# Performance work log

Hardware: AMD Instinct MI355X
Metric: run time of the kernel (lower is better)

Reference implementation:

```python
import jax, jax.numpy as jnp
import numpy as np

B, V, C, G, D, H, W, N = 1, 4, 32, 8, 8, 240, 320, 9
EPS = 1e-5  # BatchNorm3d default eps


def grid_sample(img, grid, align_corners, zeros_pad):
    # img [B,C,Hs,Ws], grid [B,Hg,Wg,2] normalized coords; mirrors torch F.grid_sample bilinear
    Bi, Ci, Hs, Ws = img.shape
    gx, gy = grid[..., 0], grid[..., 1]
    if align_corners:
        ix = (gx + 1.0) * 0.5 * (Ws - 1)
        iy = (gy + 1.0) * 0.5 * (Hs - 1)
    else:
        ix = ((gx + 1.0) * Ws - 1.0) * 0.5
        iy = ((gy + 1.0) * Hs - 1.0) * 0.5
    x0 = jnp.floor(ix)
    y0 = jnp.floor(iy)
    wx1 = ix - x0
    wy1 = iy - y0

    def corner(xi, yi, wgt):
        xc = jnp.clip(xi, 0, Ws - 1).astype(jnp.int32)
        yc = jnp.clip(yi, 0, Hs - 1).astype(jnp.int32)
        v = jax.vmap(lambda im, yy, xx: im[:, yy, xx])(img, yc, xc)  # [B,C,Hg,Wg]
        if zeros_pad:
            valid = ((xi >= 0) & (xi <= Ws - 1) & (yi >= 0) & (yi <= Hs - 1)).astype(img.dtype)
            wgt = wgt * valid
        return v * wgt[:, None]

    return (corner(x0, y0, (1 - wx1) * (1 - wy1)) + corner(x0 + 1, y0, wx1 * (1 - wy1))
            + corner(x0, y0 + 1, (1 - wx1) * wy1) + corner(x0 + 1, y0 + 1, wx1 * wy1))


def differentiable_warping(src_fea, src_proj, ref_proj, depth):
    # src_fea [B,Cf,H,W], projs [B,4,4], depth [B,D,H,W] -> [B,Cf,D,H,W]
    Bi, Cf, Hs, Ws = src_fea.shape
    Dd = depth.shape[1]
    proj = src_proj @ jnp.linalg.inv(ref_proj)
    rot, trans = proj[:, :3, :3], proj[:, :3, 3:4]
    yy, xx = jnp.meshgrid(jnp.arange(Hs, dtype=jnp.float32), jnp.arange(Ws, dtype=jnp.float32), indexing='ij')
    xyz = jnp.stack([xx.ravel(), yy.ravel(), jnp.ones(Hs * Ws, jnp.float32)], axis=0)  # [3,HW]
    rot_xyz = jnp.einsum('bij,jk->bik', rot, xyz)  # [B,3,HW]
    pxyz = rot_xyz[:, :, None, :] * depth.reshape(Bi, 1, Dd, Hs * Ws) + trans[:, :, :, None]  # [B,3,D,HW]
    neg = pxyz[:, 2] <= 1e-3
    px = jnp.where(neg, float(Ws), pxyz[:, 0])
    py = jnp.where(neg, float(Hs), pxyz[:, 1])
    pz = jnp.where(neg, 1.0, pxyz[:, 2])
    gx = (px / pz) / ((Ws - 1) / 2.0) - 1.0
    gy = (py / pz) / ((Hs - 1) / 2.0) - 1.0
    grid = jnp.stack([gx, gy], axis=-1).reshape(Bi, Dd * Hs, Ws, 2)
    grid = jax.lax.stop_gradient(grid)  # torch builds the warp grid under no_grad
    warped = grid_sample(src_fea, grid, align_corners=True, zeros_pad=True)  # [B,Cf,D*H,W]
    return warped.reshape(Bi, Cf, Dd, Hs, Ws)


def conv_bn_relu(x, w, bn):
    # 1x1x1 Conv3d (no bias) + BatchNorm3d (inference) + ReLU; x [B,Ci,D,H,W]
    y = jnp.einsum('oi,bidhw->bodhw', w, x)
    g, b, m, v = bn
    s = g / jnp.sqrt(v + EPS)
    return jax.nn.relu(y * s[:, None, None, None] + (b - m * s)[:, None, None, None])


def conv1(x, w, b):
    return jnp.einsum('oi,bidhw->bodhw', w, x) + b[:, None, None, None]


def pixel_wise_net(sim, w0, bn0, w1, bn1, w2, b2):
    y = conv_bn_relu(sim, w0, bn0)
    y = conv_bn_relu(y, w1, bn1)
    y = jax.nn.sigmoid(conv1(y, w2, b2))[:, 0]  # [B,D,H,W]
    return jnp.max(y, axis=1, keepdims=True)  # [B,1,H,W]


def _forward(ref_feature, src_features, ref_proj, src_projs, depth_sample, grid, weight,
             pw_w0, pw_bn0, pw_w1, pw_bn1, pw_w2, pw_b2,
             sn_w0, sn_bn0, sn_w1, sn_bn1, sn_w2, sn_b2):
    Bi, Cf, Hs, Ws = ref_feature.shape
    Gq = pw_w0.shape[1]
    Dd = depth_sample.shape[1]
    ref_g = ref_feature.reshape(Bi, Gq, Cf // Gq, 1, Hs, Ws)
    sim_sum = jnp.zeros((Bi, Gq, Dd, Hs, Ws), jnp.float32)
    w_sum = jnp.zeros((Bi, 1, 1, Hs, Ws), jnp.float32)
    vws = []
    for v in range(src_features.shape[0]):  # small fixed view count
        warped = differentiable_warping(src_features[v], src_projs[v], ref_proj, depth_sample)
        warped = warped.reshape(Bi, Gq, Cf // Gq, Dd, Hs, Ws)
        sim = jnp.mean(warped * ref_g, axis=2)  # [B,G,D,H,W] group correlation
        vw = pixel_wise_net(sim, pw_w0, pw_bn0, pw_w1, pw_bn1, pw_w2, pw_b2)  # [B,1,H,W]
        vws.append(vw)
        sim_sum = sim_sum + sim * vw[:, :, None]
        w_sum = w_sum + vw[:, :, None]
    x = sim_sum / w_sum
    # SimilarityNet: conv stack -> neighbor grid_sample -> adaptive weighted sum
    y = conv_bn_relu(x, sn_w0, sn_bn0)
    y = conv_bn_relu(y, sn_w1, sn_bn1)
    y = conv1(y, sn_w2, sn_b2)[:, 0]  # [B,D,H,W]
    s = grid_sample(y, grid, align_corners=False, zeros_pad=False)  # border pad, [B,D,N*H,W]
    Nn = grid.shape[1] // Hs
    s = s.reshape(Bi, Dd, Nn, Hs, Ws)
    score_vol = jnp.sum(s * weight, axis=2)  # [B,D,H,W]
    score = jax.nn.softmax(score_vol, axis=1)  # exp(log_softmax) == softmax
    depth = jnp.sum(depth_sample * score, axis=1)  # [B,H,W] (is_inverse=False)
    view_weights = jax.lax.stop_gradient(jnp.concatenate(vws, axis=1))  # [B,V,H,W]
    return depth, score, view_weights


def setup_inputs():
    key = jax.random.key(0)
    ks = jax.random.split(key, 20)
    ref_feature = jax.random.normal(ks[0], (B, C, H, W), jnp.float32)
    src_features = jax.random.normal(ks[1], (V, B, C, H, W), jnp.float32)
    f = 500.0
    K = np.array([[f, 0, W / 2.0, 0], [0, f, H / 2.0, 0], [0, 0, 1, 0], [0, 0, 0, 1]], np.float32)
    ref_proj = jnp.asarray(np.tile(K[None], (B, 1, 1)))
    sp = []
    for tx, ty in [(20.0, 0.0), (-20.0, 0.0), (0.0, 10.0), (0.0, -10.0)]:
        E = np.eye(4, dtype=np.float32)
        E[0, 3], E[1, 3] = tx, ty
        sp.append(np.tile((K @ E)[None], (B, 1, 1)))
    src_projs = jnp.asarray(np.stack(sp))
    depth_sample = jnp.sort(425.0 + 510.0 * jax.random.uniform(ks[2], (B, D, H, W), jnp.float32), axis=1)
    # evaluation neighbor grid: per-pixel +-3px learned-style offsets, align_corners=False normalization
    dx = jax.random.uniform(ks[3], (B, N, H, W), minval=-3.0, maxval=3.0)
    dy = jax.random.uniform(ks[4], (B, N, H, W), minval=-3.0, maxval=3.0)
    xs = jnp.arange(W, dtype=jnp.float32)[None, None, None, :]
    ys = jnp.arange(H, dtype=jnp.float32)[None, None, :, None]
    gx = (2.0 * (xs + dx) + 1.0) / W - 1.0
    gy = (2.0 * (ys + dy) + 1.0) / H - 1.0
    grid = jnp.stack([gx, gy], -1).reshape(B, N * H, W, 2)
    weight = jax.random.uniform(ks[5], (B, D, N, H, W), jnp.float32)  # feature*depth weight in (0,1)

    def bn(k, c):
        k1, k2, k3, k4 = jax.random.split(k, 4)
        return jnp.stack([1.0 + 0.1 * jax.random.normal(k1, (c,)), 0.1 * jax.random.normal(k2, (c,)),
                          0.01 * jax.random.normal(k3, (c,)), 1.0 + 0.1 * jax.random.uniform(k4, (c,))])

    return dict(ref_feature=ref_feature, src_features=src_features, ref_proj=ref_proj,
                src_projs=src_projs, depth_sample=depth_sample, grid=grid, weight=weight,
                pw_w0=0.1 * jax.random.normal(ks[6], (16, G)), pw_bn0=bn(ks[7], 16),
                pw_w1=0.1 * jax.random.normal(ks[8], (8, 16)), pw_bn1=bn(ks[9], 8),
                pw_w2=0.1 * jax.random.normal(ks[10], (1, 8)), pw_b2=jnp.zeros((1,), jnp.float32),
                sn_w0=0.1 * jax.random.normal(ks[11], (16, G)), sn_bn0=bn(ks[12], 16),
                sn_w1=0.1 * jax.random.normal(ks[13], (8, 16)), sn_bn1=bn(ks[14], 8),
                sn_w2=0.1 * jax.random.normal(ks[15], (1, 8)), sn_b2=jnp.zeros((1,), jnp.float32))


def reference(ref_feature, src_features, ref_proj, src_projs, depth_sample, grid, weight,
              pw_w0, pw_bn0, pw_w1, pw_bn1, pw_w2, pw_b2,
              sn_w0, sn_bn0, sn_w1, sn_bn1, sn_w2, sn_b2):
    return _forward(ref_feature, src_features, ref_proj, src_projs, depth_sample, grid, weight,
                    pw_w0, pw_bn0, pw_w1, pw_bn1, pw_w2, pw_b2,
                    sn_w0, sn_bn0, sn_w1, sn_bn1, sn_w2, sn_b2)
```

## Files before the change

kernel.cpp:

```cpp
#include <hip/hip_runtime.h>
#include <hip/hip_fp16.h>
#include <cstdint>
#include <cstddef>

#define HH 240
#define WW 320
#define HWPIX 76800
#define NVIEW 4
#define NCH 32
#define NGRP 8
#define NDEP 8
#define NNEI 9
#define SPLANE (HWPIX * NCH)

#define OFF_PROJ 0
#define OFF_PW   48
#define OFF_SN   208
#define OFF_Y    640
#define OFF_SRCT 615040
#define OFF_DEPT (OFF_SRCT + 5 * SPLANE / 2)

typedef _Float16 h2 __attribute__((ext_vector_type(2)));

__device__ __forceinline__ float fdot2_(h2 a, h2 b, float c) {
#if __has_builtin(__builtin_amdgcn_fdot2)
  return __builtin_amdgcn_fdot2(a, b, c, false);
#else
  return c + (float)a.x * (float)b.x + (float)a.y * (float)b.y;
#endif
}
__device__ __forceinline__ h2 pk_(float a, float b) {
#if __has_builtin(__builtin_amdgcn_cvt_pkrtz)
  return __builtin_bit_cast(h2, __builtin_amdgcn_cvt_pkrtz(a, b));
#else
  h2 r; r.x = (_Float16)a; r.y = (_Float16)b; return r;
#endif
}

__device__ __forceinline__ float maxd8(float x) {
  int xi = __builtin_bit_cast(int, x);
  int t = __builtin_amdgcn_mov_dpp(xi, 0xB1, 0xF, 0xF, true);
  x = fmaxf(x, __builtin_bit_cast(float, t));
  xi = __builtin_bit_cast(int, x);
  t = __builtin_amdgcn_mov_dpp(xi, 0x4E, 0xF, 0xF, true);
  x = fmaxf(x, __builtin_bit_cast(float, t));
  xi = __builtin_bit_cast(int, x);
  int a = __builtin_amdgcn_update_dpp(xi, xi, 0x124, 0xF, 0x5, false);
  int b = __builtin_amdgcn_update_dpp(a,  xi, 0x12C, 0xF, 0xA, false);
  x = fmaxf(x, __builtin_bit_cast(float, b));
  return x;
}

__device__ __forceinline__ float mlp_h(const float* __restrict__ p, const h2 x[4]) {
  const h2* w0 = (const h2*)p;
  const h2* w1 = (const h2*)(p + 64);
  const h2* w2 = (const h2*)(p + 128);
  h2 hx[8];
#pragma unroll
  for (int o = 0; o < 8; ++o) {
    float a0 = p[132 + 2 * o], a1 = p[132 + 2 * o + 1];
#pragma unroll
    for (int i = 0; i < 4; ++i) {
      a0 = fdot2_(w0[(2 * o) * 4 + i], x[i], a0);
      a1 = fdot2_(w0[(2 * o + 1) * 4 + i], x[i], a1);
    }
    hx[o] = pk_(fmaxf(a0, 0.0f), fmaxf(a1, 0.0f));
  }
  h2 hy[4];
#pragma unroll
  for (int o = 0; o < 4; ++o) {
    float a0 = p[148 + 2 * o], a1 = p[148 + 2 * o + 1];
#pragma unroll
    for (int i = 0; i < 8; ++i) {
      a0 = fdot2_(w1[(2 * o) * 8 + i], hx[i], a0);
      a1 = fdot2_(w1[(2 * o + 1) * 8 + i], hx[i], a1);
    }
    hy[o] = pk_(fmaxf(a0, 0.0f), fmaxf(a1, 0.0f));
  }
  float acc = p[156];
#pragma unroll
  for (int i = 0; i < 4; ++i) acc = fdot2_(w2[i], hy[i], acc);
  return acc;
}

__global__ void k_setup(const float* __restrict__ refP, const float* __restrict__ srcP,
                        const float* __restrict__ pw0, const float* __restrict__ pbn0,
                        const float* __restrict__ pw1, const float* __restrict__ pbn1,
                        const float* __restrict__ pw2, const float* __restrict__ pb2,
                        const float* __restrict__ sw0, const float* __restrict__ sbn0,
                        const float* __restrict__ sw1, const float* __restrict__ sbn1,
                        const float* __restrict__ sw2, const float* __restrict__ sb2,
                        float* __restrict__ ws) {
  int tid = threadIdx.x;
  if (tid == 578) {
    float a[4][8];
    for (int i = 0; i < 4; ++i)
      for (int j = 0; j < 4; ++j) { a[i][j] = refP[i * 4 + j]; a[i][4 + j] = (i == j) ? 1.0f : 0.0f; }
    for (int c = 0; c < 4; ++c) {
      int piv = c; float best = fabsf(a[c][c]);
      for (int r = c + 1; r < 4; ++r) { float t = fabsf(a[r][c]); if (t > best) { best = t; piv = r; } }
      if (piv != c) for (int j = 0; j < 8; ++j) { float t = a[c][j]; a[c][j] = a[piv][j]; a[piv][j] = t; }
      float inv = 1.0f / a[c][c];
      for (int j = 0; j < 8; ++j) a[c][j] *= inv;
      for (int r = 0; r < 4; ++r) if (r != c) {
        float f = a[r][c];
        for (int j = 0; j < 8; ++j) a[r][j] -= f * a[c][j];
      }
    }
    for (int v = 0; v < NVIEW; ++v) {
      const float* S = srcP + v * 16;
      for (int i = 0; i < 3; ++i)
        for (int j = 0; j < 4; ++j) {
          float p = S[i*4+0]*a[0][4+j] + S[i*4+1]*a[1][4+j] + S[i*4+2]*a[2][4+j] + S[i*4+3]*a[3][4+j];
          if (j < 3) ws[v * 12 + i * 3 + j] = p;
          else       ws[v * 12 + 9 + i] = p;
        }
    }
    return;
  }
  if (tid >= 578) return;
  int k = tid / 289;
  int j = tid - k * 289;
  const float* W0 = k ? sw0 : pw0;  const float* B0 = k ? sbn0 : pbn0;
  const float* W1 = k ? sw1 : pw1;  const float* B1 = k ? sbn1 : pbn1;
  const float* W2 = k ? sw2 : pw2;  const float* B2 = k ? sb2 : pb2;
  float* p = ws + (k ? OFF_SN : OFF_PW);
  __half* w0h = (__half*)p;
  __half* w1h = (__half*)(p + 64);
  __half* w2h = (__half*)(p + 128);
  if (j < 128) {
    int o = j >> 3;
    float s = B0[o] / sqrtf(B0[48 + o] + 1e-5f);
    w0h[j] = __float2half_rn(W0[j] * s * 0.25f);
  } else if (j < 256) {
    int idx = j - 128; int o = idx >> 4;
    float s = B1[o] / sqrtf(B1[24 + o] + 1e-5f);
    w1h[idx] = __float2half_rn(W1[idx] * s);
  } else if (j < 264) {
    w2h[j - 256] = __float2half_rn(W2[j - 256]);
  } else if (j < 280) {
    int o = j - 264;
    float s = B0[o] / sqrtf(B0[48 + o] + 1e-5f);
    p[132 + o] = B0[16 + o] - B0[32 + o] * s;
  } else if (j < 288) {
    int o = j - 280;
    float s = B1[o] / sqrtf(B1[24 + o] + 1e-5f);
    p[148 + o] = B1[8 + o] - B1[16 + o] * s;
  } else {
    p[156] = B2[0];
  }
}

__global__ __launch_bounds__(256) void k_transpose(const float* __restrict__ src,
                                                   const float* __restrict__ ref,
                                                   const float* __restrict__ depthS,
                                                   __half* __restrict__ dst,
                                                   float* __restrict__ dep_t, int total) {
  int t = blockIdx.x * 256 + threadIdx.x;
  if (t >= total) return;
  const int base = 5 * HWPIX * 4;
  if (t >= base) {
    int pix = t - base;
    float4 a, b;
    a.x = depthS[0 * HWPIX + pix]; a.y = depthS[1 * HWPIX + pix];
    a.z = depthS[2 * HWPIX + pix]; a.w = depthS[3 * HWPIX + pix];
    b.x = depthS[4 * HWPIX + pix]; b.y = depthS[5 * HWPIX + pix];
    b.z = depthS[6 * HWPIX + pix]; b.w = depthS[7 * HWPIX + pix];
    float4* o = reinterpret_cast<float4*>(dep_t + (size_t)pix * NDEP);
    o[0] = a; o[1] = b;
    return;
  }
  int c8 = t & 3;
  int vp = t >> 2;
  int v = vp / HWPIX;
  int pix = vp - v * HWPIX;
  const float* s = (v < NVIEW) ? (src + ((size_t)(v * NCH + c8 * 8)) * HWPIX + pix)
                               : (ref + ((size_t)(c8 * 8)) * HWPIX + pix);
  union { h2 h[4]; float4 f; } u;
  u.h[0] = pk_(s[0],         s[HWPIX]);
  u.h[1] = pk_(s[2 * HWPIX], s[3 * HWPIX]);
  u.h[2] = pk_(s[4 * HWPIX], s[5 * HWPIX]);
  u.h[3] = pk_(s[6 * HWPIX], s[7 * HWPIX]);
  reinterpret_cast<float4*>(dst + (size_t)vp * NCH)[c8] = u.f;
}

__device__ __forceinline__ void tap_f16(const __half* __restrict__ p, float wtf,
                                        h2 wp[16], bool first) {
  _Float16 wh = (_Float16)wtf;
  h2 wt2 = h2{wh, wh};
  const float4* q = reinterpret_cast<const float4*>(p);
#pragma unroll
  for (int i = 0; i < 4; ++i) {
    union { float4 f; h2 h[4]; } u; u.f = q[i];
#pragma unroll
    for (int c = 0; c < 4; ++c) {
      if (first) wp[4 * i + c] = u.h[c] * wt2;
      else       wp[4 * i + c] += u.h[c] * wt2;
    }
  }
}

template <int MODE>
__global__ __launch_bounds__(256) void k_main(
    const float* __restrict__ ref, const float* __restrict__ src,
    const __half* __restrict__ srcT,
    const float* __restrict__ depthS, const float* __restrict__ dep_t,
    const float* __restrict__ wsc,
    float* __restrict__ ybuf, float* __restrict__ outVW) {
  int t = blockIdx.x * 256 + threadIdx.x;
  int d = t & 7;
  int pix = t >> 3;
  int h = pix / WW;
  int w = pix - h * WW;
  float fx = (float)w, fy = (float)h;

  h2 rc[16];
  float rcf[(MODE == 0) ? NCH : 1];
  if (MODE == 1) {
    const float4* rp = reinterpret_cast<const float4*>(srcT + (size_t)NVIEW * SPLANE + (size_t)pix * NCH);
#pragma unroll
    for (int i = 0; i < 4; ++i) {
      union { float4 f; h2 h[4]; } u; u.f = rp[i];
      rc[4*i] = u.h[0]; rc[4*i+1] = u.h[1]; rc[4*i+2] = u.h[2]; rc[4*i+3] = u.h[3];
    }
  } else {
#pragma unroll
    for (int c = 0; c < NCH; ++c) rcf[c] = ref[c * HWPIX + pix];
  }
  float dep = (MODE == 1) ? dep_t[(size_t)pix * NDEP + d] : depthS[d * HWPIX + pix];

  float ssum[NGRP];
#pragma unroll
  for (int g = 0; g < NGRP; ++g) ssum[g] = 0.0f;
  float wsum = 0.0f;

#pragma unroll 1
  for (int v = 0; v < NVIEW; ++v) {
    const float* pr = wsc + v * 12;
    float rx = fmaf(pr[0], fx, fmaf(pr[1], fy, pr[2]));
    float ry = fmaf(pr[3], fx, fmaf(pr[4], fy, pr[5]));
    float rz = fmaf(pr[6], fx, fmaf(pr[7], fy, pr[8]));
    float pz_ = fmaf(rz, dep, pr[11]);
    bool neg = (pz_ <= 0.001f);
    float px_ = neg ? (float)WW : fmaf(rx, dep, pr[9]);
    float py_ = neg ? (float)HH : fmaf(ry, dep, pr[10]);
    float rpz = neg ? 1.0f : __fdividef(1.0f, pz_);
    float ix = px_ * rpz;
    float iy = py_ * rpz;
    float x0f = floorf(ix), y0f = floorf(iy);
    float wx1 = ix - x0f, wy1 = iy - y0f;
    float wx0 = 1.0f - wx1, wy0 = 1.0f - wy1;
    float x1f = x0f + 1.0f, y1f = y0f + 1.0f;
    float vx0 = (x0f >= 0.0f && x0f <= (float)(WW - 1)) ? 1.0f : 0.0f;
    float vx1 = (x1f >= 0.0f && x1f <= (float)(WW - 1)) ? 1.0f : 0.0f;
    float vy0 = (y0f >= 0.0f && y0f <= (float)(HH - 1)) ? 1.0f : 0.0f;
    float vy1 = (y1f >= 0.0f && y1f <= (float)(HH - 1)) ? 1.0f : 0.0f;
    int xa = (int)fminf(fmaxf(x0f, 0.0f), (float)(WW - 1));
    int xb = (int)fminf(fmaxf(x1f, 0.0f), (float)(WW - 1));
    int ya = (int)fminf(fmaxf(y0f, 0.0f), (float)(HH - 1));
    int yb = (int)fminf(fmaxf(y1f, 0.0f), (float)(HH - 1));
    float w00 = wx0 * wy0 * vx0 * vy0;
    float w01 = wx1 * wy0 * vx1 * vy0;
    float w10 = wx0 * wy1 * vx0 * vy1;
    float w11 = wx1 * wy1 * vx1 * vy1;

    float simf[NGRP];
    if (MODE == 1) {
      const __half* vbase = srcT + (size_t)v * SPLANE;
      h2 wp[16];
      tap_f16(vbase + (size_t)(ya * WW + xa) * NCH, w00, wp, true);
      tap_f16(vbase + (size_t)(ya * WW + xb) * NCH, w01, wp, false);
      tap_f16(vbase + (size_t)(yb * WW + xa) * NCH, w10, wp, false);
      tap_f16(vbase + (size_t)(yb * WW + xb) * NCH, w11, wp, false);
#pragma unroll
      for (int g = 0; g < NGRP; ++g)
        simf[g] = fdot2_(wp[2*g+1], rc[2*g+1], fdot2_(wp[2*g], rc[2*g], 0.0f));
    } else {
      const float* base = src + (size_t)v * NCH * HWPIX;
      const float* p00 = base + ya * WW + xa;
      const float* p01 = base + ya * WW + xb;
      const float* p10 = base + yb * WW + xa;
      const float* p11 = base + yb * WW + xb;
#pragma unroll
      for (int g = 0; g < NGRP; ++g) {
        float acc = 0.0f;
#pragma unroll
        for (int cc = 0; cc < 4; ++cc) {
          size_t o = (size_t)(g * 4 + cc) * HWPIX;
          float wv = w00 * p00[o] + w01 * p01[o] + w10 * p10[o] + w11 * p11[o];
          acc = fmaf(wv, rcf[g * 4 + cc], acc);
        }
        simf[g] = acc;
      }
    }

    h2 x[4];
#pragma unroll
    for (int i = 0; i < 4; ++i) x[i] = pk_(simf[2*i], simf[2*i+1]);
    float sc = mlp_h(wsc + OFF_PW, x);
    sc = maxd8(sc);
    float vw = __fdividef(1.0f, 1.0f + __expf(-sc));
#pragma unroll
    for (int g = 0; g < NGRP; ++g) ssum[g] = fmaf(simf[g], vw, ssum[g]);
    wsum += vw;
    if (d == 0) outVW[v * HWPIX + pix] = vw;
  }

  float rw = __fdividef(1.0f, wsum);
  h2 xg[4];
#pragma unroll
  for (int i = 0; i < 4; ++i) xg[i] = pk_(ssum[2*i] * rw, ssum[2*i+1] * rw);
  float yv = mlp_h(wsc + OFF_SN, xg);
  ybuf[pix * NDEP + d] = yv;
}

__global__ __launch_bounds__(256) void k_score(
    const float* __restrict__ grid, const float* __restrict__ weight,
    const float* __restrict__ depthS, const float* __restrict__ dep_t,
    const float* __restrict__ ybuf, float* __restrict__ out, int useDT) {
  int pix = blockIdx.x * 256 + threadIdx.x;
  int h = pix / WW;
  int w = pix - h * WW;
  float sv[NDEP];
#pragma unroll
  for (int d = 0; d < NDEP; ++d) sv[d] = 0.0f;

#pragma unroll 1
  for (int n = 0; n < NNEI; ++n) {
    int gi = ((n * HH + h) * WW + w) * 2;
    float gx = grid[gi], gy = grid[gi + 1];
    float ix = ((gx + 1.0f) * (float)WW - 1.0f) * 0.5f;
    float iy = ((gy + 1.0f) * (float)HH - 1.0f) * 0.5f;
    float x0f = floorf(ix), y0f = floorf(iy);
    float wx1 = ix - x0f, wy1 = iy - y0f;
    float wx0 = 1.0f - wx1, wy0 = 1.0f - wy1;
    int xa = (int)fminf(fmaxf(x0f, 0.0f), (float)(WW - 1));
    int xb = (int)fminf(fmaxf(x0f + 1.0f, 0.0f), (float)(WW - 1));
    int ya = (int)fminf(fmaxf(y0f, 0.0f), (float)(HH - 1));
    int yb2 = (int)fminf(fmaxf(y0f + 1.0f, 0.0f), (float)(HH - 1));
    const float4* p00 = reinterpret_cast<const float4*>(ybuf + (size_t)(ya * WW + xa) * NDEP);
    const float4* p01 = reinterpret_cast<const float4*>(ybuf + (size_t)(ya * WW + xb) * NDEP);
    const float4* p10 = reinterpret_cast<const float4*>(ybuf + (size_t)(yb2 * WW + xa) * NDEP);
    const float4* p11 = reinterpret_cast<const float4*>(ybuf + (size_t)(yb2 * WW + xb) * NDEP);
    float4 a00 = p00[0], b00 = p00[1];
    float4 a01 = p01[0], b01 = p01[1];
    float4 a10 = p10[0], b10 = p10[1];
    float4 a11 = p11[0], b11 = p11[1];
    const float* v00 = (const float*)&a00;
    const float* v01 = (const float*)&a01;
    const float* v10 = (const float*)&a10;
    const float* v11 = (const float*)&a11;
    const float* u00 = (const float*)&b00;
    const float* u01 = (const float*)&b01;
    const float* u10 = (const float*)&b10;
    const float* u11 = (const float*)&b11;
#pragma unroll
    for (int d = 0; d < NDEP; ++d) {
      float c00 = (d < 4) ? v00[d] : u00[d - 4];
      float c01 = (d < 4) ? v01[d] : u01[d - 4];
      float c10 = (d < 4) ? v10[d] : u10[d - 4];
      float c11 = (d < 4) ? v11[d] : u11[d - 4];
      float s = wy0 * fmaf(wx0, c00, wx1 * c01) + wy1 * fmaf(wx0, c10, wx1 * c11);
      float wn = weight[((size_t)(d * NNEI + n) * HH + h) * WW + w];
      sv[d] = fmaf(s, wn, sv[d]);
    }
  }
  float m = sv[0];
#pragma unroll
  for (int d = 1; d < NDEP; ++d) m = fmaxf(m, sv[d]);
  float e[NDEP], s8 = 0.0f;
#pragma unroll
  for (int d = 0; d < NDEP; ++d) { e[d] = __expf(sv[d] - m); s8 += e[d]; }
  float r = __fdividef(1.0f, s8);
  float dpv[NDEP];
  if (useDT) {
    const float4* dp4 = reinterpret_cast<const float4*>(dep_t + (size_t)pix * NDEP);
    float4 da = dp4[0], db = dp4[1];
    dpv[0]=da.x; dpv[1]=da.y; dpv[2]=da.z; dpv[3]=da.w;
    dpv[4]=db.x; dpv[5]=db.y; dpv[6]=db.z; dpv[7]=db.w;
  } else {
#pragma unroll
    for (int d = 0; d < NDEP; ++d) dpv[d] = depthS[d * HWPIX + pix];
  }
  float dp = 0.0f;
#pragma unroll
  for (int d = 0; d < NDEP; ++d) {
    float sc = e[d] * r;
    out[HWPIX + d * HWPIX + pix] = sc;
    dp = fmaf(dpv[d], sc, dp);
  }
  out[pix] = dp;
}

extern "C" void kernel_launch(void* const* d_in, const int* in_sizes, int n_in,
                              void* d_out, int out_size, void* d_ws, size_t ws_size,
                              hipStream_t stream) {
  const float* ref    = (const float*)d_in[0];
  const float* src    = (const float*)d_in[1];
  const float* refP   = (const float*)d_in[2];
  const float* srcP   = (const float*)d_in[3];
  const float* depthS = (const float*)d_in[4];
  const float* grid   = (const float*)d_in[5];
  const float* weight = (const float*)d_in[6];
  float* out = (float*)d_out;
  float* ws  = (float*)d_ws;
  __half* srcT = (__half*)(ws + OFF_SRCT);
  float* dep_t = ws + OFF_DEPT;

  size_t need = ((size_t)OFF_DEPT + (size_t)NDEP * HWPIX) * 4;
  int mode = (ws_size >= need) ? 1 : 0;

  k_setup<<<1, 640, 0, stream>>>(refP, srcP,
                                 (const float*)d_in[7], (const float*)d_in[8],
                                 (const float*)d_in[9], (const float*)d_in[10],
                                 (const float*)d_in[11], (const float*)d_in[12],
                                 (const float*)d_in[13], (const float*)d_in[14],
                                 (const float*)d_in[15], (const float*)d_in[16],
                                 (const float*)d_in[17], (const float*)d_in[18], ws);
  if (mode == 1) {
    int total = 5 * HWPIX * 4 + HWPIX;
    k_transpose<<<(total + 255) / 256, 256, 0, stream>>>(src, ref, depthS, srcT, dep_t, total);
    k_main<1><<<(HWPIX * 8) / 256, 256, 0, stream>>>(ref, src, srcT, depthS, dep_t, ws,
                                                     ws + OFF_Y, out + 9 * HWPIX);
  } else {
    k_main<0><<<(HWPIX * 8) / 256, 256, 0, stream>>>(ref, src, srcT, depthS, dep_t, ws,
                                                     ws + OFF_Y, out + 9 * HWPIX);
  }
  k_score<<<HWPIX / 256, 256, 0, stream>>>(grid, weight, depthS, dep_t, ws + OFF_Y, out, mode);
}
```

Before: 93.31 us.

## Run per-pixel MLPs on MFMA and merge setup into transpose kernel

Replaces the scalar fdot2-based three-layer MLPs (pixel-wise view weight net and similarity net) with 32x32x16 f16 MFMA instructions. Weight fragments are pre-laid out in the workspace, and half-wave shuffles exchange activations between lanes. The setup kernel is folded into the transpose kernel as an extra block, which removes one launch. The fallback non-transposed path is dropped, so a large workspace is now assumed. The new layout adds shuffle and select overhead, and the MFMA tiles are mostly padding.

```diff
diff --git a/kernel.cpp b/kernel.cpp
--- a/kernel.cpp
+++ b/kernel.cpp
@@ -13,14 +13,14 @@
 #define NNEI 9
 #define SPLANE (HWPIX * NCH)
 
-#define OFF_PROJ 0
-#define OFF_PW   48
-#define OFF_SN   208
-#define OFF_Y    640
-#define OFF_SRCT 615040
-#define OFF_DEPT (OFF_SRCT + 5 * SPLANE / 2)
+#define OFF_TAB 64
+#define OFF_Y    4096
+#define OFF_SRCT 618496
+#define OFF_DEPT 6762496
 
 typedef _Float16 h2 __attribute__((ext_vector_type(2)));
+typedef __fp16  h8v __attribute__((ext_vector_type(8)));
+typedef float f32x16 __attribute__((ext_vector_type(16)));
 
 __device__ __forceinline__ float fdot2_(h2 a, h2 b, float c) {
 #if __has_builtin(__builtin_amdgcn_fdot2)
@@ -35,6 +35,13 @@
 #else
   h2 r; r.x = (_Float16)a; r.y = (_Float16)b; return r;
 #endif
+}
+__device__ __forceinline__ float pkf_(float a, float b) {
+  return __builtin_bit_cast(float, pk_(a, b));
+}
+
+__device__ __forceinline__ f32x16 mfma_(h8v a, h8v b, f32x16 c) {
+  return __builtin_amdgcn_mfma_f32_32x32x16_f16(a, b, c, 0, 0, 0);
 }
 
 __device__ __forceinline__ float maxd8(float x) {
@@ -51,113 +58,145 @@
   return x;
 }
 
-__device__ __forceinline__ float mlp_h(const float* __restrict__ p, const h2 x[4]) {
-  const h2* w0 = (const h2*)p;
-  const h2* w1 = (const h2*)(p + 64);
-  const h2* w2 = (const h2*)(p + 128);
-  h2 hx[8];
-#pragma unroll
-  for (int o = 0; o < 8; ++o) {
-    float a0 = p[132 + 2 * o], a1 = p[132 + 2 * o + 1];
-#pragma unroll
-    for (int i = 0; i < 4; ++i) {
-      a0 = fdot2_(w0[(2 * o) * 4 + i], x[i], a0);
-      a1 = fdot2_(w0[(2 * o + 1) * 4 + i], x[i], a1);
-    }
-    hx[o] = pk_(fmaxf(a0, 0.0f), fmaxf(a1, 0.0f));
-  }
-  h2 hy[4];
-#pragma unroll
-  for (int o = 0; o < 4; ++o) {
-    float a0 = p[148 + 2 * o], a1 = p[148 + 2 * o + 1];
-#pragma unroll
-    for (int i = 0; i < 8; ++i) {
-      a0 = fdot2_(w1[(2 * o) * 8 + i], hx[i], a0);
-      a1 = fdot2_(w1[(2 * o + 1) * 8 + i], hx[i], a1);
-    }
-    hy[o] = pk_(fmaxf(a0, 0.0f), fmaxf(a1, 0.0f));
-  }
-  float acc = p[156];
-#pragma unroll
-  for (int i = 0; i < 4; ++i) acc = fdot2_(w2[i], hy[i], acc);
-  return acc;
-}
-
-__global__ void k_setup(const float* __restrict__ refP, const float* __restrict__ srcP,
-                        const float* __restrict__ pw0, const float* __restrict__ pbn0,
-                        const float* __restrict__ pw1, const float* __restrict__ pbn1,
-                        const float* __restrict__ pw2, const float* __restrict__ pb2,
-                        const float* __restrict__ sw0, const float* __restrict__ sbn0,
-                        const float* __restrict__ sw1, const float* __restrict__ sbn1,
-                        const float* __restrict__ sw2, const float* __restrict__ sb2,
-                        float* __restrict__ ws) {
-  int tid = threadIdx.x;
-  if (tid == 578) {
-    float a[4][8];
-    for (int i = 0; i < 4; ++i)
-      for (int j = 0; j < 4; ++j) { a[i][j] = refP[i * 4 + j]; a[i][4 + j] = (i == j) ? 1.0f : 0.0f; }
-    for (int c = 0; c < 4; ++c) {
-      int piv = c; float best = fabsf(a[c][c]);
-      for (int r = c + 1; r < 4; ++r) { float t = fabsf(a[r][c]); if (t > best) { best = t; piv = r; } }
-      if (piv != c) for (int j = 0; j < 8; ++j) { float t = a[c][j]; a[c][j] = a[piv][j]; a[piv][j] = t; }
-      float inv = 1.0f / a[c][c];
-      for (int j = 0; j < 8; ++j) a[c][j] *= inv;
-      for (int r = 0; r < 4; ++r) if (r != c) {
-        float f = a[r][c];
-        for (int j = 0; j < 8; ++j) a[r][j] -= f * a[c][j];
+__device__ __forceinline__ float mlp_mfma(float4 x4, h8v w0f, h8v w1f,
+                                          float4 b1s, float4 w2s, float b2v,
+                                          bool lo) {
+  f32x16 Z = {};
+  float4 xsw;
+  xsw.x = __shfl_xor(x4.x, 32, 64);
+  xsw.y = __shfl_xor(x4.y, 32, 64);
+  xsw.z = __shfl_xor(x4.z, 32, 64);
+  xsw.w = __shfl_xor(x4.w, 32, 64);
+  float4 cst;
+  cst.x = __builtin_bit_cast(float, 0x00003C00u);
+  cst.y = 0.0f; cst.z = 0.0f; cst.w = 0.0f;
+  float4 blo, bhi;
+  blo.x = lo ? x4.x : cst.x;  blo.y = lo ? x4.y : cst.y;
+  blo.z = lo ? x4.z : cst.z;  blo.w = lo ? x4.w : cst.w;
+  bhi.x = lo ? xsw.x : cst.x; bhi.y = lo ? xsw.y : cst.y;
+  bhi.z = lo ? xsw.z : cst.z; bhi.w = lo ? xsw.w : cst.w;
+
+  float yv0 = 0.0f, yv1 = 0.0f;
+#pragma unroll
+  for (int bb = 0; bb < 2; ++bb) {
+    float4 bin = bb ? bhi : blo;
+    f32x16 acc = mfma_(w0f, __builtin_bit_cast(h8v, bin), Z);
+    float dw0 = pkf_(fmaxf(acc[0], 0.f), fmaxf(acc[1], 0.f));
+    float dw1 = pkf_(fmaxf(acc[2], 0.f), fmaxf(acc[3], 0.f));
+    float dw2 = pkf_(fmaxf(acc[4], 0.f), fmaxf(acc[5], 0.f));
+    float dw3 = pkf_(fmaxf(acc[6], 0.f), fmaxf(acc[7], 0.f));
+    float s0 = __shfl_xor(dw0, 32, 64);
+    float s1 = __shfl_xor(dw1, 32, 64);
+    float s2 = __shfl_xor(dw2, 32, 64);
+    float s3 = __shfl_xor(dw3, 32, 64);
+    float4 bf;
+    bf.x = lo ? dw0 : s2;
+    bf.y = lo ? dw1 : s3;
+    bf.z = lo ? s0 : dw2;
+    bf.w = lo ? s1 : dw3;
+    f32x16 a2 = mfma_(w1f, __builtin_bit_cast(h8v, bf), Z);
+    float p = fmaxf(a2[0] + b1s.x, 0.f) * w2s.x;
+    p = fmaf(fmaxf(a2[1] + b1s.y, 0.f), w2s.y, p);
+    p = fmaf(fmaxf(a2[2] + b1s.z, 0.f), w2s.z, p);
+    p = fmaf(fmaxf(a2[3] + b1s.w, 0.f), w2s.w, p);
+    p += __shfl_xor(p, 32, 64);
+    if (bb) yv1 = p + b2v; else yv0 = p + b2v;
+  }
+  return lo ? yv0 : yv1;
+}
+
+__global__ __launch_bounds__(256) void k_prep(
+    const float* __restrict__ src, const float* __restrict__ ref,
+    const float* __restrict__ depthS,
+    __half* __restrict__ dst, float* __restrict__ dep_t,
+    const float* __restrict__ refP, const float* __restrict__ srcP,
+    const float* __restrict__ pw0, const float* __restrict__ pbn0,
+    const float* __restrict__ pw1, const float* __restrict__ pbn1,
+    const float* __restrict__ pw2, const float* __restrict__ pb2,
+    const float* __restrict__ sw0, const float* __restrict__ sbn0,
+    const float* __restrict__ sw1, const float* __restrict__ sbn1,
+    const float* __restrict__ sw2, const float* __restrict__ sb2,
+    float* __restrict__ ws, int nTransBlocks) {
+  if ((int)blockIdx.x == nTransBlocks) {
+    int tid = threadIdx.x;
+    if (tid < 128) {
+      int net = tid >> 6;
+      int l = tid & 63;
+      int n = l & 31;
+      int hi = l >> 5;
+      const float* W0 = net ? sw0 : pw0;  const float* B0 = net ? sbn0 : pbn0;
+      const float* W1 = net ? sw1 : pw1;  const float* B1 = net ? sbn1 : pbn1;
+      const float* W2 = net ? sw2 : pw2;
+      float* base = ws + OFF_TAB + net * 1024;
+      float4 r;
+      if (hi == 0 && n < 16) {
+        float s = B0[n] / sqrtf(B0[48 + n] + 1e-5f) * 0.25f;
+        r.x = pkf_(W0[n * 8 + 0] * s, W0[n * 8 + 1] * s);
+        r.y = pkf_(W0[n * 8 + 2] * s, W0[n * 8 + 3] * s);
+        r.z = pkf_(W0[n * 8 + 4] * s, W0[n * 8 + 5] * s);
+        r.w = pkf_(W0[n * 8 + 6] * s, W0[n * 8 + 7] * s);
+      } else if (hi == 1 && n < 16) {
+        float s = B0[n] / sqrtf(B0[48 + n] + 1e-5f);
+        float b0f = B0[16 + n] - B0[32 + n] * s;
+        r.x = pkf_(b0f, 0.f); r.y = 0.f; r.z = 0.f; r.w = 0.f;
+      } else { r.x = r.y = r.z = r.w = 0.f; }
+      ((float4*)(base))[l] = r;
+      float4 q;
+      if (n < 8) {
+        float s = B1[n] / sqrtf(B1[24 + n] + 1e-5f);
+        int o = n * 16 + 8 * hi;
+        q.x = pkf_(W1[o + 0] * s, W1[o + 1] * s);
+        q.y = pkf_(W1[o + 2] * s, W1[o + 3] * s);
+        q.z = pkf_(W1[o + 4] * s, W1[o + 5] * s);
+        q.w = pkf_(W1[o + 6] * s, W1[o + 7] * s);
+      } else { q.x = q.y = q.z = q.w = 0.f; }
+      ((float4*)(base + 256))[l] = q;
+      float4 b;
+      {
+        float bb[4];
+        for (int rr = 0; rr < 4; ++rr) {
+          int o = rr + 4 * hi;
+          float s = B1[o] / sqrtf(B1[24 + o] + 1e-5f);
+          bb[rr] = B1[8 + o] - B1[16 + o] * s;
+        }
+        b.x = bb[0]; b.y = bb[1]; b.z = bb[2]; b.w = bb[3];
+      }
+      ((float4*)(base + 512))[l] = b;
+      float4 w2v;
+      w2v.x = W2[0 + 4 * hi]; w2v.y = W2[1 + 4 * hi];
+      w2v.z = W2[2 + 4 * hi]; w2v.w = W2[3 + 4 * hi];
+      ((float4*)(base + 768))[l] = w2v;
+    } else if (tid == 128) {
+      ws[62] = pb2[0];
+      ws[63] = sb2[0];
+    } else if (tid == 129) {
+      float a[4][8];
+      for (int i = 0; i < 4; ++i)
+        for (int j = 0; j < 4; ++j) { a[i][j] = refP[i * 4 + j]; a[i][4 + j] = (i == j) ? 1.0f : 0.0f; }
+      for (int c = 0; c < 4; ++c) {
+        int piv = c; float best = fabsf(a[c][c]);
+        for (int r2 = c + 1; r2 < 4; ++r2) { float t = fabsf(a[r2][c]); if (t > best) { best = t; piv = r2; } }
+        if (piv != c) for (int j = 0; j < 8; ++j) { float t = a[c][j]; a[c][j] = a[piv][j]; a[piv][j] = t; }
+        float inv = 1.0f / a[c][c];
+        for (int j = 0; j < 8; ++j) a[c][j] *= inv;
+        for (int r2 = 0; r2 < 4; ++r2) if (r2 != c) {
+          float f = a[r2][c];
+          for (int j = 0; j < 8; ++j) a[r2][j] -= f * a[c][j];
+        }
+      }
+      for (int v = 0; v < NVIEW; ++v) {
+        const float* S = srcP + v * 16;
+        for (int i = 0; i < 3; ++i)
+          for (int j = 0; j < 4; ++j) {
+            float p = S[i*4+0]*a[0][4+j] + S[i*4+1]*a[1][4+j] + S[i*4+2]*a[2][4+j] + S[i*4+3]*a[3][4+j];
+            if (j < 3) ws[v * 12 + i * 3 + j] = p;
+            else       ws[v * 12 + 9 + i] = p;
+          }
       }
     }
-    for (int v = 0; v < NVIEW; ++v) {
-      const float* S = srcP + v * 16;
-      for (int i = 0; i < 3; ++i)
-        for (int j = 0; j < 4; ++j) {
-          float p = S[i*4+0]*a[0][4+j] + S[i*4+1]*a[1][4+j] + S[i*4+2]*a[2][4+j] + S[i*4+3]*a[3][4+j];
-          if (j < 3) ws[v * 12 + i * 3 + j] = p;
-          else       ws[v * 12 + 9 + i] = p;
-        }
-    }
     return;
   }
-  if (tid >= 578) return;
-  int k = tid / 289;
-  int j = tid - k * 289;
-  const float* W0 = k ? sw0 : pw0;  const float* B0 = k ? sbn0 : pbn0;
-  const float* W1 = k ? sw1 : pw1;  const float* B1 = k ? sbn1 : pbn1;
-  const float* W2 = k ? sw2 : pw2;  const float* B2 = k ? sb2 : pb2;
-  float* p = ws + (k ? OFF_SN : OFF_PW);
-  __half* w0h = (__half*)p;
-  __half* w1h = (__half*)(p + 64);
-  __half* w2h = (__half*)(p + 128);
-  if (j < 128) {
-    int o = j >> 3;
-    float s = B0[o] / sqrtf(B0[48 + o] + 1e-5f);
-    w0h[j] = __float2half_rn(W0[j] * s * 0.25f);
-  } else if (j < 256) {
-    int idx = j - 128; int o = idx >> 4;
-    float s = B1[o] / sqrtf(B1[24 + o] + 1e-5f);
-    w1h[idx] = __float2half_rn(W1[idx] * s);
-  } else if (j < 264) {
-    w2h[j - 256] = __float2half_rn(W2[j - 256]);
-  } else if (j < 280) {
-    int o = j - 264;
-    float s = B0[o] / sqrtf(B0[48 + o] + 1e-5f);
-    p[132 + o] = B0[16 + o] - B0[32 + o] * s;
-  } else if (j < 288) {
-    int o = j - 280;
-    float s = B1[o] / sqrtf(B1[24 + o] + 1e-5f);
-    p[148 + o] = B1[8 + o] - B1[16 + o] * s;
-  } else {
-    p[156] = B2[0];
-  }
-}
-
-__global__ __launch_bounds__(256) void k_transpose(const float* __restrict__ src,
-                                                   const float* __restrict__ ref,
-                                                   const float* __restrict__ depthS,
-                                                   __half* __restrict__ dst,
-                                                   float* __restrict__ dep_t, int total) {
   int t = blockIdx.x * 256 + threadIdx.x;
-  if (t >= total) return;
   const int base = 5 * HWPIX * 4;
   if (t >= base) {
     int pix = t - base;
@@ -200,34 +239,37 @@
   }
 }
 
-template <int MODE>
 __global__ __launch_bounds__(256) void k_main(
-    const float* __restrict__ ref, const float* __restrict__ src,
-    const __half* __restrict__ srcT,
-    const float* __restrict__ depthS, const float* __restrict__ dep_t,
+    const __half* __restrict__ srcT, const float* __restrict__ dep_t,
     const float* __restrict__ wsc,
     float* __restrict__ ybuf, float* __restrict__ outVW) {
   int t = blockIdx.x * 256 + threadIdx.x;
+  int lane = threadIdx.x & 63;
+  bool lo = lane < 32;
   int d = t & 7;
   int pix = t >> 3;
   int h = pix / WW;
   int w = pix - h * WW;
   float fx = (float)w, fy = (float)h;
 
+  const h8v* Tw0p = (const h8v*)(wsc + OFF_TAB);
+  const h8v* Tw1p = (const h8v*)(wsc + OFF_TAB + 256);
+  h8v w0f_pw = Tw0p[lane];
+  h8v w1f_pw = Tw1p[lane];
+  float4 b1s_pw = ((const float4*)(wsc + OFF_TAB + 512))[lane];
+  float4 w2s_pw = ((const float4*)(wsc + OFF_TAB + 768))[lane];
+  float b2_pw = wsc[62];
+
   h2 rc[16];
-  float rcf[(MODE == 0) ? NCH : 1];
-  if (MODE == 1) {
+  {
     const float4* rp = reinterpret_cast<const float4*>(srcT + (size_t)NVIEW * SPLANE + (size_t)pix * NCH);
 #pragma unroll
     for (int i = 0; i < 4; ++i) {
       union { float4 f; h2 h[4]; } u; u.f = rp[i];
       rc[4*i] = u.h[0]; rc[4*i+1] = u.h[1]; rc[4*i+2] = u.h[2]; rc[4*i+3] = u.h[3];
     }
-  } else {
-#pragma unroll
-    for (int c = 0; c < NCH; ++c) rcf[c] = ref[c * HWPIX + pix];
-  }
-  float dep = (MODE == 1) ? dep_t[(size_t)pix * NDEP + d] : depthS[d * HWPIX + pix];
+  }
+  float dep = dep_t[(size_t)pix * NDEP + d];
 
   float ssum[NGRP];
 #pragma unroll
@@ -265,7 +307,7 @@
     float w11 = wx1 * wy1 * vx1 * vy1;
 
     float simf[NGRP];
-    if (MODE == 1) {
+    {
       const __half* vbase = srcT + (size_t)v * SPLANE;
       h2 wp[16];
       tap_f16(vbase + (size_t)(ya * WW + xa) * NCH, w00, wp, true);
@@ -275,29 +317,14 @@
 #pragma unroll
       for (int g = 0; g < NGRP; ++g)
         simf[g] = fdot2_(wp[2*g+1], rc[2*g+1], fdot2_(wp[2*g], rc[2*g], 0.0f));
-    } else {
-      const float* base = src + (size_t)v * NCH * HWPIX;
-      const float* p00 = base + ya * WW + xa;
-      const float* p01 = base + ya * WW + xb;
-      const float* p10 = base + yb * WW + xa;
-      const float* p11 = base + yb * WW + xb;
-#pragma unroll
-      for (int g = 0; g < NGRP; ++g) {
-        float acc = 0.0f;
-#pragma unroll
-        for (int cc = 0; cc < 4; ++cc) {
-          size_t o = (size_t)(g * 4 + cc) * HWPIX;
-          float wv = w00 * p00[o] + w01 * p01[o] + w10 * p10[o] + w11 * p11[o];
-          acc = fmaf(wv, rcf[g * 4 + cc], acc);
-        }
-        simf[g] = acc;
-      }
     }
 
-    h2 x[4];
-#pragma unroll
-    for (int i = 0; i < 4; ++i) x[i] = pk_(simf[2*i], simf[2*i+1]);
-    float sc = mlp_h(wsc + OFF_PW, x);
+    float4 xp;
+    xp.x = pkf_(simf[0], simf[1]);
+    xp.y = pkf_(simf[2], simf[3]);
+    xp.z = pkf_(simf[4], simf[5]);
+    xp.w = pkf_(simf[6], simf[7]);
+    float sc = mlp_mfma(xp, w0f_pw, w1f_pw, b1s_pw, w2s_pw, b2_pw, lo);
     sc = maxd8(sc);
     float vw = __fdividef(1.0f, 1.0f + __expf(-sc));
 #pragma unroll
@@ -307,17 +334,24 @@
   }
 
   float rw = __fdividef(1.0f, wsum);
-  h2 xg[4];
-#pragma unroll
-  for (int i = 0; i < 4; ++i) xg[i] = pk_(ssum[2*i] * rw, ssum[2*i+1] * rw);
-  float yv = mlp_h(wsc + OFF_SN, xg);
+  float4 xg;
+  xg.x = pkf_(ssum[0] * rw, ssum[1] * rw);
+  xg.y = pkf_(ssum[2] * rw, ssum[3] * rw);
+  xg.z = pkf_(ssum[4] * rw, ssum[5] * rw);
+  xg.w = pkf_(ssum[6] * rw, ssum[7] * rw);
+  h8v w0f_sn = ((const h8v*)(wsc + OFF_TAB + 1024))[lane];
+  h8v w1f_sn = ((const h8v*)(wsc + OFF_TAB + 1024 + 256))[lane];
+  float4 b1s_sn = ((const float4*)(wsc + OFF_TAB + 1024 + 512))[lane];
+  float4 w2s_sn = ((const float4*)(wsc + OFF_TAB + 1024 + 768))[lane];
+  float b2_sn = wsc[63];
+  float yv = mlp_mfma(xg, w0f_sn, w1f_sn, b1s_sn, w2s_sn, b2_sn, lo);
   ybuf[pix * NDEP + d] = yv;
 }
 
 __global__ __launch_bounds__(256) void k_score(
     const float* __restrict__ grid, const float* __restrict__ weight,
-    const float* __restrict__ depthS, const float* __restrict__ dep_t,
-    const float* __restrict__ ybuf, float* __restrict__ out, int useDT) {
+    const float* __restrict__ dep_t, const float* __restrict__ ybuf,
+    float* __restrict__ out) {
   int pix = blockIdx.x * 256 + threadIdx.x;
   int h = pix / WW;
   int w = pix - h * WW;
@@ -372,16 +406,9 @@
 #pragma unroll
   for (int d = 0; d < NDEP; ++d) { e[d] = __expf(sv[d] - m); s8 += e[d]; }
   float r = __fdividef(1.0f, s8);
-  float dpv[NDEP];
-  if (useDT) {
-    const float4* dp4 = reinterpret_cast<const float4*>(dep_t + (size_t)pix * NDEP);
-    float4 da = dp4[0], db = dp4[1];
-    dpv[0]=da.x; dpv[1]=da.y; dpv[2]=da.z; dpv[3]=da.w;
-    dpv[4]=db.x; dpv[5]=db.y; dpv[6]=db.z; dpv[7]=db.w;
-  } else {
-#pragma unroll
-    for (int d = 0; d < NDEP; ++d) dpv[d] = depthS[d * HWPIX + pix];
-  }
+  const float4* dp4 = reinterpret_cast<const float4*>(dep_t + (size_t)pix * NDEP);
+  float4 da = dp4[0], db = dp4[1];
+  float dpv[NDEP] = {da.x, da.y, da.z, da.w, db.x, db.y, db.z, db.w};
   float dp = 0.0f;
 #pragma unroll
   for (int d = 0; d < NDEP; ++d) {
@@ -407,24 +434,18 @@
   __half* srcT = (__half*)(ws + OFF_SRCT);
   float* dep_t = ws + OFF_DEPT;
 
-  size_t need = ((size_t)OFF_DEPT + (size_t)NDEP * HWPIX) * 4;
-  int mode = (ws_size >= need) ? 1 : 0;
-
-  k_setup<<<1, 640, 0, stream>>>(refP, srcP,
-                                 (const float*)d_in[7], (const float*)d_in[8],
-                                 (const float*)d_in[9], (const float*)d_in[10],
-                                 (const float*)d_in[11], (const float*)d_in[12],
-                                 (const float*)d_in[13], (const float*)d_in[14],
-                                 (const float*)d_in[15], (const float*)d_in[16],
-                                 (const float*)d_in[17], (const float*)d_in[18], ws);
-  if (mode == 1) {
-    int total = 5 * HWPIX * 4 + HWPIX;
-    k_transpose<<<(total + 255) / 256, 256, 0, stream>>>(src, ref, depthS, srcT, dep_t, total);
-    k_main<1><<<(HWPIX * 8) / 256, 256, 0, stream>>>(ref, src, srcT, depthS, dep_t, ws,
-                                                     ws + OFF_Y, out + 9 * HWPIX);
-  } else {
-    k_main<0><<<(HWPIX * 8) / 256, 256, 0, stream>>>(ref, src, srcT, depthS, dep_t, ws,
-                                                     ws + OFF_Y, out + 9 * HWPIX);
-  }
-  k_score<<<HWPIX / 256, 256, 0, stream>>>(grid, weight, depthS, dep_t, ws + OFF_Y, out, mode);
-}
+  int transThreads = 5 * HWPIX * 4 + HWPIX;
+  int nTransBlocks = transThreads / 256;
+
+  k_prep<<<nTransBlocks + 1, 256, 0, stream>>>(
+      src, ref, depthS, srcT, dep_t, refP, srcP,
+      (const float*)d_in[7],  (const float*)d_in[8],
+      (const float*)d_in[9],  (const float*)d_in[10],
+      (const float*)d_in[11], (const float*)d_in[12],
+      (const float*)d_in[13], (const float*)d_in[14],
+      (const float*)d_in[15], (const float*)d_in[16],
+      (const float*)d_in[17], (const float*)d_in[18],
+      ws, nTransBlocks);
+  k_main<<<(HWPIX * 8) / 256, 256, 0, stream>>>(srcT, dep_t, ws, ws + OFF_Y, out + 9 * HWPIX);
+  k_score<<<HWPIX / 256, 256, 0, stream>>>(grid, weight, dep_t, ws + OFF_Y, out);
+}
```

Measured after the change: 89.82 us. 3.7% less time.
